# Optimization experiments

Measured on AMD Instinct MI355X. Metric: run time of the kernel, lower is better.

## Reference

```python
import jax, jax.numpy as jnp
import numpy as np

TOKENS, HIDDEN = 2048, 1024
N_EXPERTS, INTER, TOPK = 8, 2816, 2
RENORMALIZE = True


def setup_inputs() -> dict:
    key = jax.random.key(0)
    k1, k2, k3, k4 = jax.random.split(key, 4)
    x = jax.random.normal(k1, (TOKENS, HIDDEN), dtype=jnp.float32)
    gating_output = jax.random.normal(k2, (TOKENS, N_EXPERTS), dtype=jnp.float32)
    # stacked gate_proj+up_proj per expert: [E, 2*I, H]
    w1 = jax.random.normal(k3, (N_EXPERTS, 2 * INTER, HIDDEN), dtype=jnp.float32) * 0.02
    # down_proj per expert: [E, H, I]
    w2 = jax.random.normal(k4, (N_EXPERTS, HIDDEN, INTER), dtype=jnp.float32) * 0.02
    return {"x": x, "gating_output": gating_output, "w1": w1, "w2": w2}


def _moe(x, gating_output, w1, w2):
    # fused_topk: softmax over router logits, then top-k, then renormalize
    probs = jax.nn.softmax(gating_output, axis=-1)              # [T, E]
    topk_w, topk_ids = jax.lax.top_k(probs, TOPK)                # [T, K]
    if RENORMALIZE:
        topk_w = topk_w / jnp.sum(topk_w, axis=-1, keepdims=True)
    # fused_experts: gate/up proj -> SiLU(gate)*up -> down proj, per expert
    h = jnp.einsum('th,eih->tei', x, w1)                         # [T, E, 2I]
    gate, up = h[..., :INTER], h[..., INTER:]
    act = jax.nn.silu(gate) * up                                 # [T, E, I]
    out_e = jnp.einsum('tei,ehi->teh', act, w2)                  # [T, E, H]
    # combine: gather selected experts and weight them
    sel = jnp.take_along_axis(out_e, topk_ids[:, :, None], axis=1)  # [T, K, H]
    return jnp.sum(sel * topk_w[:, :, None].astype(sel.dtype), axis=1)  # [T, H]


def reference(x, gating_output, w1, w2):
    return _moe(x, gating_output, w1, w2)
```

## Files before the change

### kernel.cpp

```cpp
#include <hip/hip_runtime.h>
#include <hip/hip_bf16.h>

#define TOKENS 2048
#define HIDDEN 1024
#define NEXP   8
#define INTER  2816
#define N1     5632
#define ROWCAP 5120
#define MT     40
#define NT1    44
#define NT2    8
#define SPLITK 2

typedef __attribute__((ext_vector_type(8))) short short8;
typedef __attribute__((ext_vector_type(4))) float f32x4;

typedef unsigned int __attribute__((address_space(1))) as1_uint;
typedef unsigned int __attribute__((address_space(3))) as3_uint;

__device__ __forceinline__ void gload16(const void* g, void* l) {
  __builtin_amdgcn_global_load_lds((const as1_uint*)g, (as3_uint*)l, 16, 0, 0);
}

__device__ __forceinline__ unsigned short f2bf(float f) {
  unsigned u = __float_as_uint(f);
  u += 0x7fff + ((u >> 16) & 1);
  return (unsigned short)(u >> 16);
}
__device__ __forceinline__ float bf2f(unsigned short h) {
  return __uint_as_float(((unsigned)h) << 16);
}
__device__ __forceinline__ unsigned short bfs(float x) {
  __hip_bfloat16 h = __float2bfloat16(x);
  return *reinterpret_cast<unsigned short*>(&h);
}
__device__ __forceinline__ short8 pack8(f32x4 lo, f32x4 hi) {
  short8 o;
  o[0] = (short)bfs(lo[0]); o[1] = (short)bfs(lo[1]); o[2] = (short)bfs(lo[2]); o[3] = (short)bfs(lo[3]);
  o[4] = (short)bfs(hi[0]); o[5] = (short)bfs(hi[1]); o[6] = (short)bfs(hi[2]); o[7] = (short)bfs(hi[3]);
  return o;
}

__global__ void k_routing(const float* __restrict__ gate, int* __restrict__ ctrl,
                          int* __restrict__ tkid, float* __restrict__ tkw) {
  int t = blockIdx.x * blockDim.x + threadIdx.x;
  if (t >= TOKENS) return;
  float l[8];
#pragma unroll
  for (int i = 0; i < 8; i++) l[i] = gate[t * 8 + i];
  int i0 = 0; float m0 = l[0];
#pragma unroll
  for (int i = 1; i < 8; i++) if (l[i] > m0) { m0 = l[i]; i0 = i; }
  int i1 = -1; float m1 = -3.4e38f;
#pragma unroll
  for (int i = 0; i < 8; i++) if (i != i0 && l[i] > m1) { m1 = l[i]; i1 = i; }
  float e  = __expf(m1 - m0);
  float w0 = 1.f / (1.f + e);
  float w1 = e / (1.f + e);
  tkid[2 * t] = i0; tkid[2 * t + 1] = i1;
  tkw[2 * t] = w0;  tkw[2 * t + 1] = w1;
  atomicAdd(&ctrl[i0], 1);
  atomicAdd(&ctrl[i1], 1);
}

__global__ void k_base(int* ctrl) {
  if (threadIdx.x == 0) {
    int a = 0;
    for (int e = 0; e < 8; e++) { ctrl[16 + e] = a; a += ((ctrl[e] + 127) >> 7) << 7; }
  }
}

__global__ void k_fill(int* __restrict__ ctrl, const int* __restrict__ tkid,
                       int* __restrict__ rtok, int* __restrict__ trow) {
  int t = blockIdx.x * blockDim.x + threadIdx.x;
  if (t >= TOKENS) return;
#pragma unroll
  for (int k = 0; k < 2; k++) {
    int e = tkid[2 * t + k];
    int pos = atomicAdd(&ctrl[8 + e], 1);
    int row = ctrl[16 + e] + pos;
    rtok[row] = t;
    trow[2 * t + k] = row;
  }
}

__global__ void k_gather(const float* __restrict__ x, const int* __restrict__ ctrl,
                         const int* __restrict__ rtok, unsigned short* __restrict__ Abf) {
  int row = blockIdx.x;
  int e = -1, local = 0;
  for (int i = 0; i < 8; i++) {
    int b = ctrl[16 + i], p = ((ctrl[i] + 127) >> 7) << 7;
    if (row >= b && row < b + p) { e = i; local = row - b; break; }
  }
  if (e < 0) return;
  int tid = threadIdx.x;
  unsigned short* dst = Abf + (size_t)row * HIDDEN;
  if (local < ctrl[e]) {
    int t = rtok[row];
    float4 v = ((const float4*)(x + (size_t)t * HIDDEN))[tid];
    ushort4 o; o.x = f2bf(v.x); o.y = f2bf(v.y); o.z = f2bf(v.z); o.w = f2bf(v.w);
    ((ushort4*)dst)[tid] = o;
  } else {
    ushort4 z; z.x = 0; z.y = 0; z.z = 0; z.w = 0;
    ((ushort4*)dst)[tid] = z;
  }
}

__device__ __forceinline__ int tile_lookup(const int* ctrl, int mt, int* ml) {
  int a0 = 0;
  for (int i = 0; i < 8; i++) {
    int pt = (ctrl[i] + 127) >> 7;
    if (mt < a0 + pt) { *ml = mt - a0; return i; }
    a0 += pt;
  }
  return -1;
}

__global__ __launch_bounds__(256, 3) void k_gemm1(const float* __restrict__ w1,
    const unsigned short* __restrict__ Abf, unsigned short* __restrict__ act,
    const int* __restrict__ ctrl) {
  union __align__(16) LdsU {
    struct { unsigned char A[16384]; unsigned char Bf[32768]; } st;
    unsigned short hb[128 * 132];
  };
  __shared__ LdsU lds;
  int bid = blockIdx.x;
  int wg = (bid & 7) * (NT1 * MT / 8) + (bid >> 3);
  int nt = wg / MT, mt = wg % MT;
  int ml; int e = tile_lookup(ctrl, mt, &ml);
  if (e < 0) return;
  int tid = threadIdx.x, lane = tid & 63, wid = tid >> 6, wr = wid >> 1, wc = wid & 1;
  int rbase = ctrl[16 + e] + ml * 128;
  const unsigned char* Ab = (const unsigned char*)(Abf + (size_t)rbase * HIDDEN);
  const unsigned char* Bw = (const unsigned char*)(w1 + (size_t)e * N1 * HIDDEN);
  int l3 = lane >> 3, l4 = lane >> 4, l15 = lane & 15;
  int swzA = ((lane & 7) ^ l3) << 4;

  unsigned aoff[4], boff[8];
#pragma unroll
  for (int i = 0; i < 4; i++) {
    int g = wid * 4 + i;
    aoff[i] = (unsigned)(g * 8 + l3) * (HIDDEN * 2) + swzA;
  }
#pragma unroll
  for (int i = 0; i < 8; i++) {
    int r = (wid * 8 + i) * 4 + l4;
    int grow = (r < 64) ? nt * 64 + r : INTER + nt * 64 + (r - 64);
    boff[i] = (unsigned)grow * (HIDDEN * 4) + ((l15 ^ (r & 15)) << 4);
  }

  f32x4 acc[4][4];
  f32x4 zero = {0.f, 0.f, 0.f, 0.f};
#pragma unroll
  for (int i = 0; i < 4; i++)
#pragma unroll
    for (int j = 0; j < 4; j++) acc[i][j] = zero;

  for (int kk = 0; kk < HIDDEN / 64; ++kk) {
#pragma unroll
    for (int i = 0; i < 4; i++)
      gload16(Ab + (size_t)aoff[i] + kk * 128, &lds.st.A[(wid * 4 + i) * 1024]);
#pragma unroll
    for (int i = 0; i < 8; i++)
      gload16(Bw + (size_t)boff[i] + kk * 256, &lds.st.Bf[(wid * 8 + i) * 1024]);
    __syncthreads();
#pragma unroll
    for (int ks = 0; ks < 2; ++ks) {
      short8 a[4], b[4];
#pragma unroll
      for (int mi = 0; mi < 4; mi++) {
        int row = wr * 64 + mi * 16 + l15;
        int koff = ks * 64 + (l4 << 4);
        a[mi] = *(const short8*)&lds.st.A[row * 128 + (koff ^ ((row & 7) << 4))];
      }
#pragma unroll
      for (int ni = 0; ni < 4; ni++) {
        int r = wc * 64 + ni * 16 + l15;
        int c = ks * 8 + l4 * 2;
        f32x4 lo = *(const f32x4*)&lds.st.Bf[r * 256 + ((c ^ (r & 15)) << 4)];
        f32x4 hi = *(const f32x4*)&lds.st.Bf[r * 256 + (((c + 1) ^ (r & 15)) << 4)];
        b[ni] = pack8(lo, hi);
      }
#pragma unroll
      for (int mi = 0; mi < 4; mi++)
#pragma unroll
        for (int ni = 0; ni < 4; ni++)
          acc[mi][ni] = __builtin_amdgcn_mfma_f32_16x16x32_bf16(a[mi], b[ni], acc[mi][ni], 0, 0, 0);
    }
    __syncthreads();
  }
#pragma unroll
  for (int mi = 0; mi < 4; mi++)
#pragma unroll
    for (int ni = 0; ni < 4; ni++)
#pragma unroll
      for (int r = 0; r < 4; r++) {
        int row = wr * 64 + mi * 16 + (l4 << 2) + r;
        int col = wc * 64 + ni * 16 + l15;
        lds.hb[row * 132 + col] = f2bf(acc[mi][ni][r]);
      }
  __syncthreads();
  {
    int r = tid >> 1, ch = (tid & 1) * 32;
    unsigned short* orow = act + (size_t)(rbase + r) * INTER + nt * 64 + ch;
    const unsigned short* hrow = &lds.hb[r * 132];
#pragma unroll
    for (int j = 0; j < 32; j += 4) {
      ushort4 o;
#pragma unroll
      for (int q = 0; q < 4; q++) {
        float g = bf2f(hrow[ch + j + q]);
        float u = bf2f(hrow[64 + ch + j + q]);
        float s = g / (1.f + __expf(-g));
        ((unsigned short*)&o)[q] = f2bf(s * u);
      }
      *(ushort4*)(orow + j) = o;
    }
  }
}

__global__ __launch_bounds__(256, 3) void k_gemm2(const float* __restrict__ w2,
    const unsigned short* __restrict__ act, float* __restrict__ Pb,
    const int* __restrict__ ctrl) {
  struct __align__(16) Lds2 { unsigned char A[16384]; unsigned char Bf[32768]; };
  __shared__ Lds2 lds;
  int bid = blockIdx.x;
  int wg = (bid & 7) * (NT2 * MT * SPLITK / 8) + (bid >> 3);
  int mt = wg % MT;
  int p = wg / MT;
  int z = p & 1, nt = p >> 1;
  int ml; int e = tile_lookup(ctrl, mt, &ml);
  if (e < 0) return;
  int tid = threadIdx.x, lane = tid & 63, wid = tid >> 6, wr = wid >> 1, wc = wid & 1;
  int rbase = ctrl[16 + e] + ml * 128;
  const int KST = (INTER / 64) / SPLITK;
  const unsigned char* Ab = (const unsigned char*)(act + (size_t)rbase * INTER) + (size_t)z * KST * 128;
  const unsigned char* Bw = (const unsigned char*)(w2 + (size_t)e * HIDDEN * INTER) + (size_t)z * KST * 256;
  int l3 = lane >> 3, l4 = lane >> 4, l15 = lane & 15;
  int swzA = ((lane & 7) ^ l3) << 4;

  unsigned aoff[4], boff[8];
#pragma unroll
  for (int i = 0; i < 4; i++) {
    int g = wid * 4 + i;
    aoff[i] = (unsigned)(g * 8 + l3) * (INTER * 2) + swzA;
  }
#pragma unroll
  for (int i = 0; i < 8; i++) {
    int r = (wid * 8 + i) * 4 + l4;
    boff[i] = (unsigned)(nt * 128 + r) * (INTER * 4) + ((l15 ^ (r & 15)) << 4);
  }

  f32x4 acc[4][4];
  f32x4 zero = {0.f, 0.f, 0.f, 0.f};
#pragma unroll
  for (int i = 0; i < 4; i++)
#pragma unroll
    for (int j = 0; j < 4; j++) acc[i][j] = zero;

  for (int s = 0; s < KST; ++s) {
#pragma unroll
    for (int i = 0; i < 4; i++)
      gload16(Ab + (size_t)aoff[i] + s * 128, &lds.A[(wid * 4 + i) * 1024]);
#pragma unroll
    for (int i = 0; i < 8; i++)
      gload16(Bw + (size_t)boff[i] + s * 256, &lds.Bf[(wid * 8 + i) * 1024]);
    __syncthreads();
#pragma unroll
    for (int ks = 0; ks < 2; ++ks) {
      short8 a[4], b[4];
#pragma unroll
      for (int mi = 0; mi < 4; mi++) {
        int row = wr * 64 + mi * 16 + l15;
        int koff = ks * 64 + (l4 << 4);
        a[mi] = *(const short8*)&lds.A[row * 128 + (koff ^ ((row & 7) << 4))];
      }
#pragma unroll
      for (int ni = 0; ni < 4; ni++) {
        int r = wc * 64 + ni * 16 + l15;
        int c = ks * 8 + l4 * 2;
        f32x4 lo = *(const f32x4*)&lds.Bf[r * 256 + ((c ^ (r & 15)) << 4)];
        f32x4 hi = *(const f32x4*)&lds.Bf[r * 256 + (((c + 1) ^ (r & 15)) << 4)];
        b[ni] = pack8(lo, hi);
      }
#pragma unroll
      for (int mi = 0; mi < 4; mi++)
#pragma unroll
        for (int ni = 0; ni < 4; ni++)
          acc[mi][ni] = __builtin_amdgcn_mfma_f32_16x16x32_bf16(a[mi], b[ni], acc[mi][ni], 0, 0, 0);
    }
    __syncthreads();
  }
  float* P = Pb + (size_t)z * ROWCAP * HIDDEN;
#pragma unroll
  for (int mi = 0; mi < 4; mi++)
#pragma unroll
    for (int ni = 0; ni < 4; ni++) {
      int col = nt * 128 + wc * 64 + ni * 16 + l15;
#pragma unroll
      for (int r = 0; r < 4; r++) {
        int row = rbase + wr * 64 + mi * 16 + (l4 << 2) + r;
        P[(size_t)row * HIDDEN + col] = acc[mi][ni][r];
      }
    }
}

__global__ void k_finish(const float* __restrict__ Pb,
                         const int* __restrict__ trow, const float* __restrict__ tkw,
                         float* __restrict__ out) {
  int t = blockIdx.x, c = threadIdx.x;
  const float* P0 = Pb;
  const float* P1 = Pb + (size_t)ROWCAP * HIDDEN;
  int r0 = trow[2 * t], r1 = trow[2 * t + 1];
  float w0 = tkw[2 * t], w1 = tkw[2 * t + 1];
  float4 a0 = ((const float4*)(P0 + (size_t)r0 * HIDDEN))[c];
  float4 b0 = ((const float4*)(P1 + (size_t)r0 * HIDDEN))[c];
  float4 a1 = ((const float4*)(P0 + (size_t)r1 * HIDDEN))[c];
  float4 b1 = ((const float4*)(P1 + (size_t)r1 * HIDDEN))[c];
  float4 o;
  o.x = w0 * (a0.x + b0.x) + w1 * (a1.x + b1.x);
  o.y = w0 * (a0.y + b0.y) + w1 * (a1.y + b1.y);
  o.z = w0 * (a0.z + b0.z) + w1 * (a1.z + b1.z);
  o.w = w0 * (a0.w + b0.w) + w1 * (a1.w + b1.w);
  ((float4*)(out + (size_t)t * HIDDEN))[c] = o;
}

extern "C" void kernel_launch(void* const* d_in, const int* in_sizes, int n_in,
                              void* d_out, int out_size, void* d_ws, size_t ws_size,
                              hipStream_t stream) {
  const float* x      = (const float*)d_in[0];
  const float* gating = (const float*)d_in[1];
  const float* w1     = (const float*)d_in[2];
  const float* w2     = (const float*)d_in[3];
  float* out = (float*)d_out;
  char* ws = (char*)d_ws;

  int*   ctrl = (int*)ws;
  int*   tkid = (int*)(ws + 4096);
  float* tkw  = (float*)(ws + 24576);
  int*   rtok = (int*)(ws + 45056);
  int*   trow = (int*)(ws + 73728);
  size_t off_Abf = 131072;
  size_t off_act = off_Abf + (size_t)ROWCAP * HIDDEN * 2;
  size_t off_P   = off_act + (size_t)ROWCAP * INTER * 2;
  unsigned short* Abf  = (unsigned short*)(ws + off_Abf);
  unsigned short* actb = (unsigned short*)(ws + off_act);
  float* Pb = (float*)(ws + off_P);

  hipMemsetAsync(ws, 0, 1024, stream);

  k_routing<<<TOKENS / 256, 256, 0, stream>>>(gating, ctrl, tkid, tkw);
  k_base<<<1, 64, 0, stream>>>(ctrl);
  k_fill<<<TOKENS / 256, 256, 0, stream>>>(ctrl, tkid, rtok, trow);
  k_gather<<<ROWCAP, 256, 0, stream>>>(x, ctrl, rtok, Abf);
  k_gemm1<<<NT1 * MT, 256, 0, stream>>>(w1, Abf, actb, ctrl);
  k_gemm2<<<NT2 * MT * SPLITK, 256, 0, stream>>>(w2, actb, Pb, ctrl);
  k_finish<<<TOKENS, 256, 0, stream>>>(Pb, trow, tkw, out);
}
```

Baseline: 239.2 us.

## Use 256-row M tiles with 512 threads and double-buffered LDS in expert GEMMs

Both expert GEMMs now use 256-row M tiles with 8 waves per block, and expert row padding is raised to 256 to match (ROWCAP 6144, MT 24). The K loop is restructured into a two-stage LDS ping-pong, so the next slab's global-to-LDS loads are issued while MFMAs run on the current one. This aims to hide load latency and to reuse each weight tile across twice as many rows. In exchange, the larger padding adds wasted rows of compute, and the 128KB LDS footprint limits each CU to one block, so occupancy drops.

```diff
diff --git a/kernel.cpp b/kernel.cpp
--- a/kernel.cpp
+++ b/kernel.cpp
@@ -6,8 +6,8 @@
 #define NEXP   8
 #define INTER  2816
 #define N1     5632
-#define ROWCAP 5120
-#define MT     40
+#define ROWCAP 6144
+#define MT     24
 #define NT1    44
 #define NT2    8
 #define SPLITK 2
@@ -66,7 +66,7 @@
 __global__ void k_base(int* ctrl) {
   if (threadIdx.x == 0) {
     int a = 0;
-    for (int e = 0; e < 8; e++) { ctrl[16 + e] = a; a += ((ctrl[e] + 127) >> 7) << 7; }
+    for (int e = 0; e < 8; e++) { ctrl[16 + e] = a; a += ((ctrl[e] + 255) >> 8) << 8; }
   }
 }
 
@@ -89,7 +89,7 @@
   int row = blockIdx.x;
   int e = -1, local = 0;
   for (int i = 0; i < 8; i++) {
-    int b = ctrl[16 + i], p = ((ctrl[i] + 127) >> 7) << 7;
+    int b = ctrl[16 + i], p = ((ctrl[i] + 255) >> 8) << 8;
     if (row >= b && row < b + p) { e = i; local = row - b; break; }
   }
   if (e < 0) return;
@@ -109,19 +109,20 @@
 __device__ __forceinline__ int tile_lookup(const int* ctrl, int mt, int* ml) {
   int a0 = 0;
   for (int i = 0; i < 8; i++) {
-    int pt = (ctrl[i] + 127) >> 7;
+    int pt = (ctrl[i] + 255) >> 8;
     if (mt < a0 + pt) { *ml = mt - a0; return i; }
     a0 += pt;
   }
   return -1;
 }
 
-__global__ __launch_bounds__(256, 3) void k_gemm1(const float* __restrict__ w1,
+__global__ __launch_bounds__(512, 2) void k_gemm1(const float* __restrict__ w1,
     const unsigned short* __restrict__ Abf, unsigned short* __restrict__ act,
     const int* __restrict__ ctrl) {
   union __align__(16) LdsU {
-    struct { unsigned char A[16384]; unsigned char Bf[32768]; } st;
-    unsigned short hb[128 * 132];
+    struct { unsigned char A0[32768]; unsigned char Bf0[32768];
+             unsigned char A1[32768]; unsigned char Bf1[32768]; } st;
+    unsigned short hb[256 * 132];
   };
   __shared__ LdsU lds;
   int bid = blockIdx.x;
@@ -130,21 +131,21 @@
   int ml; int e = tile_lookup(ctrl, mt, &ml);
   if (e < 0) return;
   int tid = threadIdx.x, lane = tid & 63, wid = tid >> 6, wr = wid >> 1, wc = wid & 1;
-  int rbase = ctrl[16 + e] + ml * 128;
+  int rbase = ctrl[16 + e] + ml * 256;
   const unsigned char* Ab = (const unsigned char*)(Abf + (size_t)rbase * HIDDEN);
   const unsigned char* Bw = (const unsigned char*)(w1 + (size_t)e * N1 * HIDDEN);
   int l3 = lane >> 3, l4 = lane >> 4, l15 = lane & 15;
   int swzA = ((lane & 7) ^ l3) << 4;
 
-  unsigned aoff[4], boff[8];
+  unsigned aoff[4], boff[4];
 #pragma unroll
   for (int i = 0; i < 4; i++) {
     int g = wid * 4 + i;
     aoff[i] = (unsigned)(g * 8 + l3) * (HIDDEN * 2) + swzA;
   }
 #pragma unroll
-  for (int i = 0; i < 8; i++) {
-    int r = (wid * 8 + i) * 4 + l4;
+  for (int i = 0; i < 4; i++) {
+    int r = (wid * 4 + i) * 4 + l4;
     int grow = (r < 64) ? nt * 64 + r : INTER + nt * 64 + (r - 64);
     boff[i] = (unsigned)grow * (HIDDEN * 4) + ((l15 ^ (r & 15)) << 4);
   }
@@ -156,39 +157,48 @@
 #pragma unroll
     for (int j = 0; j < 4; j++) acc[i][j] = zero;
 
-  for (int kk = 0; kk < HIDDEN / 64; ++kk) {
-#pragma unroll
-    for (int i = 0; i < 4; i++)
-      gload16(Ab + (size_t)aoff[i] + kk * 128, &lds.st.A[(wid * 4 + i) * 1024]);
-#pragma unroll
-    for (int i = 0; i < 8; i++)
-      gload16(Bw + (size_t)boff[i] + kk * 256, &lds.st.Bf[(wid * 8 + i) * 1024]);
+#define STG1(kk, Ad, Bd) do {                                                        \
+  _Pragma("unroll") for (int i = 0; i < 4; i++)                                      \
+    gload16(Ab + (size_t)aoff[i] + (kk) * 128, &(Ad)[(wid * 4 + i) * 1024]);         \
+  _Pragma("unroll") for (int i = 0; i < 4; i++)                                      \
+    gload16(Bw + (size_t)boff[i] + (kk) * 256, &(Bd)[(wid * 4 + i) * 1024]);         \
+} while (0)
+
+#define CMP1(Ad, Bd) do {                                                            \
+  _Pragma("unroll") for (int ks = 0; ks < 2; ++ks) {                                 \
+    short8 a[4], b[4];                                                               \
+    _Pragma("unroll") for (int mi = 0; mi < 4; mi++) {                               \
+      int row = wr * 64 + mi * 16 + l15;                                             \
+      int koff = ks * 64 + (l4 << 4);                                                \
+      a[mi] = *(const short8*)&(Ad)[row * 128 + (koff ^ ((row & 7) << 4))];          \
+    }                                                                                \
+    _Pragma("unroll") for (int ni = 0; ni < 4; ni++) {                               \
+      int r = wc * 64 + ni * 16 + l15;                                               \
+      int c = ks * 8 + l4 * 2;                                                       \
+      f32x4 lo = *(const f32x4*)&(Bd)[r * 256 + ((c ^ (r & 15)) << 4)];              \
+      f32x4 hi = *(const f32x4*)&(Bd)[r * 256 + (((c + 1) ^ (r & 15)) << 4)];        \
+      b[ni] = pack8(lo, hi);                                                         \
+    }                                                                                \
+    _Pragma("unroll") for (int mi = 0; mi < 4; mi++)                                 \
+      _Pragma("unroll") for (int ni = 0; ni < 4; ni++)                               \
+        acc[mi][ni] = __builtin_amdgcn_mfma_f32_16x16x32_bf16(a[mi], b[ni], acc[mi][ni], 0, 0, 0); \
+  }                                                                                  \
+} while (0)
+
+  const int NS = HIDDEN / 64;
+  STG1(0, lds.st.A0, lds.st.Bf0);
+  __syncthreads();
+  for (int s = 0; s < NS; s += 2) {
+    STG1(s + 1, lds.st.A1, lds.st.Bf1);
+    CMP1(lds.st.A0, lds.st.Bf0);
     __syncthreads();
-#pragma unroll
-    for (int ks = 0; ks < 2; ++ks) {
-      short8 a[4], b[4];
-#pragma unroll
-      for (int mi = 0; mi < 4; mi++) {
-        int row = wr * 64 + mi * 16 + l15;
-        int koff = ks * 64 + (l4 << 4);
-        a[mi] = *(const short8*)&lds.st.A[row * 128 + (koff ^ ((row & 7) << 4))];
-      }
-#pragma unroll
-      for (int ni = 0; ni < 4; ni++) {
-        int r = wc * 64 + ni * 16 + l15;
-        int c = ks * 8 + l4 * 2;
-        f32x4 lo = *(const f32x4*)&lds.st.Bf[r * 256 + ((c ^ (r & 15)) << 4)];
-        f32x4 hi = *(const f32x4*)&lds.st.Bf[r * 256 + (((c + 1) ^ (r & 15)) << 4)];
-        b[ni] = pack8(lo, hi);
-      }
-#pragma unroll
-      for (int mi = 0; mi < 4; mi++)
-#pragma unroll
-        for (int ni = 0; ni < 4; ni++)
-          acc[mi][ni] = __builtin_amdgcn_mfma_f32_16x16x32_bf16(a[mi], b[ni], acc[mi][ni], 0, 0, 0);
-    }
+    if (s + 2 < NS) STG1(s + 2, lds.st.A0, lds.st.Bf0);
+    CMP1(lds.st.A1, lds.st.Bf1);
     __syncthreads();
   }
+#undef STG1
+#undef CMP1
+
 #pragma unroll
   for (int mi = 0; mi < 4; mi++)
 #pragma unroll
@@ -219,10 +229,11 @@
   }
 }
 
-__global__ __launch_bounds__(256, 3) void k_gemm2(const float* __restrict__ w2,
+__global__ __launch_bounds__(512, 2) void k_gemm2(const float* __restrict__ w2,
     const unsigned short* __restrict__ act, float* __restrict__ Pb,
     const int* __restrict__ ctrl) {
-  struct __align__(16) Lds2 { unsigned char A[16384]; unsigned char Bf[32768]; };
+  struct __align__(16) Lds2 { unsigned char A0[32768]; unsigned char Bf0[32768];
+                              unsigned char A1[32768]; unsigned char Bf1[32768]; };
   __shared__ Lds2 lds;
   int bid = blockIdx.x;
   int wg = (bid & 7) * (NT2 * MT * SPLITK / 8) + (bid >> 3);
@@ -232,22 +243,22 @@
   int ml; int e = tile_lookup(ctrl, mt, &ml);
   if (e < 0) return;
   int tid = threadIdx.x, lane = tid & 63, wid = tid >> 6, wr = wid >> 1, wc = wid & 1;
-  int rbase = ctrl[16 + e] + ml * 128;
+  int rbase = ctrl[16 + e] + ml * 256;
   const int KST = (INTER / 64) / SPLITK;
   const unsigned char* Ab = (const unsigned char*)(act + (size_t)rbase * INTER) + (size_t)z * KST * 128;
   const unsigned char* Bw = (const unsigned char*)(w2 + (size_t)e * HIDDEN * INTER) + (size_t)z * KST * 256;
   int l3 = lane >> 3, l4 = lane >> 4, l15 = lane & 15;
   int swzA = ((lane & 7) ^ l3) << 4;
 
-  unsigned aoff[4], boff[8];
+  unsigned aoff[4], boff[4];
 #pragma unroll
   for (int i = 0; i < 4; i++) {
     int g = wid * 4 + i;
     aoff[i] = (unsigned)(g * 8 + l3) * (INTER * 2) + swzA;
   }
 #pragma unroll
-  for (int i = 0; i < 8; i++) {
-    int r = (wid * 8 + i) * 4 + l4;
+  for (int i = 0; i < 4; i++) {
+    int r = (wid * 4 + i) * 4 + l4;
     boff[i] = (unsigned)(nt * 128 + r) * (INTER * 4) + ((l15 ^ (r & 15)) << 4);
   }
 
@@ -258,39 +269,47 @@
 #pragma unroll
     for (int j = 0; j < 4; j++) acc[i][j] = zero;
 
-  for (int s = 0; s < KST; ++s) {
-#pragma unroll
-    for (int i = 0; i < 4; i++)
-      gload16(Ab + (size_t)aoff[i] + s * 128, &lds.A[(wid * 4 + i) * 1024]);
-#pragma unroll
-    for (int i = 0; i < 8; i++)
-      gload16(Bw + (size_t)boff[i] + s * 256, &lds.Bf[(wid * 8 + i) * 1024]);
+#define STG2(kk, Ad, Bd) do {                                                        \
+  _Pragma("unroll") for (int i = 0; i < 4; i++)                                      \
+    gload16(Ab + (size_t)aoff[i] + (kk) * 128, &(Ad)[(wid * 4 + i) * 1024]);         \
+  _Pragma("unroll") for (int i = 0; i < 4; i++)                                      \
+    gload16(Bw + (size_t)boff[i] + (kk) * 256, &(Bd)[(wid * 4 + i) * 1024]);         \
+} while (0)
+
+#define CMP2(Ad, Bd) do {                                                            \
+  _Pragma("unroll") for (int ks = 0; ks < 2; ++ks) {                                 \
+    short8 a[4], b[4];                                                               \
+    _Pragma("unroll") for (int mi = 0; mi < 4; mi++) {                               \
+      int row = wr * 64 + mi * 16 + l15;                                             \
+      int koff = ks * 64 + (l4 << 4);                                                \
+      a[mi] = *(const short8*)&(Ad)[row * 128 + (koff ^ ((row & 7) << 4))];          \
+    }                                                                                \
+    _Pragma("unroll") for (int ni = 0; ni < 4; ni++) {                               \
+      int r = wc * 64 + ni * 16 + l15;                                               \
+      int c = ks * 8 + l4 * 2;                                                       \
+      f32x4 lo = *(const f32x4*)&(Bd)[r * 256 + ((c ^ (r & 15)) << 4)];              \
+      f32x4 hi = *(const f32x4*)&(Bd)[r * 256 + (((c + 1) ^ (r & 15)) << 4)];        \
+      b[ni] = pack8(lo, hi);                                                         \
+    }                                                                                \
+    _Pragma("unroll") for (int mi = 0; mi < 4; mi++)                                 \
+      _Pragma("unroll") for (int ni = 0; ni < 4; ni++)                               \
+        acc[mi][ni] = __builtin_amdgcn_mfma_f32_16x16x32_bf16(a[mi], b[ni], acc[mi][ni], 0, 0, 0); \
+  }                                                                                  \
+} while (0)
+
+  STG2(0, lds.A0, lds.Bf0);
+  __syncthreads();
+  for (int s = 0; s < KST; s += 2) {
+    STG2(s + 1, lds.A1, lds.Bf1);
+    CMP2(lds.A0, lds.Bf0);
     __syncthreads();
-#pragma unroll
-    for (int ks = 0; ks < 2; ++ks) {
-      short8 a[4], b[4];
-#pragma unroll
-      for (int mi = 0; mi < 4; mi++) {
-        int row = wr * 64 + mi * 16 + l15;
-        int koff = ks * 64 + (l4 << 4);
-        a[mi] = *(const short8*)&lds.A[row * 128 + (koff ^ ((row & 7) << 4))];
-      }
-#pragma unroll
-      for (int ni = 0; ni < 4; ni++) {
-        int r = wc * 64 + ni * 16 + l15;
-        int c = ks * 8 + l4 * 2;
-        f32x4 lo = *(const f32x4*)&lds.Bf[r * 256 + ((c ^ (r & 15)) << 4)];
-        f32x4 hi = *(const f32x4*)&lds.Bf[r * 256 + (((c + 1) ^ (r & 15)) << 4)];
-        b[ni] = pack8(lo, hi);
-      }
-#pragma unroll
-      for (int mi = 0; mi < 4; mi++)
-#pragma unroll
-        for (int ni = 0; ni < 4; ni++)
-          acc[mi][ni] = __builtin_amdgcn_mfma_f32_16x16x32_bf16(a[mi], b[ni], acc[mi][ni], 0, 0, 0);
-    }
+    if (s + 2 < KST) STG2(s + 2, lds.A0, lds.Bf0);
+    CMP2(lds.A1, lds.Bf1);
     __syncthreads();
   }
+#undef STG2
+#undef CMP2
+
   float* P = Pb + (size_t)z * ROWCAP * HIDDEN;
 #pragma unroll
   for (int mi = 0; mi < 4; mi++)
@@ -353,7 +372,7 @@
   k_base<<<1, 64, 0, stream>>>(ctrl);
   k_fill<<<TOKENS / 256, 256, 0, stream>>>(ctrl, tkid, rtok, trow);
   k_gather<<<ROWCAP, 256, 0, stream>>>(x, ctrl, rtok, Abf);
-  k_gemm1<<<NT1 * MT, 256, 0, stream>>>(w1, Abf, actb, ctrl);
-  k_gemm2<<<NT2 * MT * SPLITK, 256, 0, stream>>>(w2, actb, Pb, ctrl);
+  k_gemm1<<<NT1 * MT, 512, 0, stream>>>(w1, Abf, actb, ctrl);
+  k_gemm2<<<NT2 * MT * SPLITK, 512, 0, stream>>>(w2, actb, Pb, ctrl);
   k_finish<<<TOKENS, 256, 0, stream>>>(Pb, trow, tkw, out);
 }
```

After: 277.4 us. 16.0% more time.

## Pre-convert expert weights to bf16 before the expert GEMMs

Applied to the files above, without the earlier changes.

Adds a grid-stride conversion kernel that turns w1 and w2 from fp32 to bf16 in workspace on every call. Both GEMMs then load bf16 B tiles directly with the same swizzled layout as A, so the per-MFMA fp32-to-bf16 packing disappears. B tiles shrink to half the LDS, which allows launch bounds of 4 blocks per CU. The cost is an extra full pass over all weights each call: a fp32 read plus a bf16 write. The split-K partial buffer is aliased onto the w1 bf16 region, which gemm1 has already finished reading by the time gemm2 writes there.

```diff
diff --git a/kernel.cpp b/kernel.cpp
--- a/kernel.cpp
+++ b/kernel.cpp
@@ -30,15 +30,18 @@
 __device__ __forceinline__ float bf2f(unsigned short h) {
   return __uint_as_float(((unsigned)h) << 16);
 }
-__device__ __forceinline__ unsigned short bfs(float x) {
-  __hip_bfloat16 h = __float2bfloat16(x);
-  return *reinterpret_cast<unsigned short*>(&h);
-}
-__device__ __forceinline__ short8 pack8(f32x4 lo, f32x4 hi) {
-  short8 o;
-  o[0] = (short)bfs(lo[0]); o[1] = (short)bfs(lo[1]); o[2] = (short)bfs(lo[2]); o[3] = (short)bfs(lo[3]);
-  o[4] = (short)bfs(hi[0]); o[5] = (short)bfs(hi[1]); o[6] = (short)bfs(hi[2]); o[7] = (short)bfs(hi[3]);
-  return o;
+
+__global__ void k_conv(const float* __restrict__ src, unsigned short* __restrict__ dst, int n8) {
+  int i = blockIdx.x * blockDim.x + threadIdx.x;
+  int stride = gridDim.x * blockDim.x;
+  for (; i < n8; i += stride) {
+    float4 a = ((const float4*)src)[2 * i];
+    float4 b = ((const float4*)src)[2 * i + 1];
+    union { ushort us[8]; uint4 v; } o;
+    o.us[0] = f2bf(a.x); o.us[1] = f2bf(a.y); o.us[2] = f2bf(a.z); o.us[3] = f2bf(a.w);
+    o.us[4] = f2bf(b.x); o.us[5] = f2bf(b.y); o.us[6] = f2bf(b.z); o.us[7] = f2bf(b.w);
+    ((uint4*)dst)[i] = o.v;
+  }
 }
 
 __global__ void k_routing(const float* __restrict__ gate, int* __restrict__ ctrl,
@@ -116,11 +119,11 @@
   return -1;
 }
 
-__global__ __launch_bounds__(256, 3) void k_gemm1(const float* __restrict__ w1,
+__global__ __launch_bounds__(256, 4) void k_gemm1b(const unsigned short* __restrict__ w1b,
     const unsigned short* __restrict__ Abf, unsigned short* __restrict__ act,
     const int* __restrict__ ctrl) {
   union __align__(16) LdsU {
-    struct { unsigned char A[16384]; unsigned char Bf[32768]; } st;
+    struct { unsigned char A[16384]; unsigned char B[16384]; } st;
     unsigned short hb[128 * 132];
   };
   __shared__ LdsU lds;
@@ -132,21 +135,18 @@
   int tid = threadIdx.x, lane = tid & 63, wid = tid >> 6, wr = wid >> 1, wc = wid & 1;
   int rbase = ctrl[16 + e] + ml * 128;
   const unsigned char* Ab = (const unsigned char*)(Abf + (size_t)rbase * HIDDEN);
-  const unsigned char* Bw = (const unsigned char*)(w1 + (size_t)e * N1 * HIDDEN);
+  const unsigned char* Bb = (const unsigned char*)(w1b + (size_t)e * N1 * HIDDEN);
   int l3 = lane >> 3, l4 = lane >> 4, l15 = lane & 15;
-  int swzA = ((lane & 7) ^ l3) << 4;
-
-  unsigned aoff[4], boff[8];
+  int swz = ((lane & 7) ^ l3) << 4;
+
+  unsigned aoff[4], boff[4];
 #pragma unroll
   for (int i = 0; i < 4; i++) {
     int g = wid * 4 + i;
-    aoff[i] = (unsigned)(g * 8 + l3) * (HIDDEN * 2) + swzA;
-  }
-#pragma unroll
-  for (int i = 0; i < 8; i++) {
-    int r = (wid * 8 + i) * 4 + l4;
-    int grow = (r < 64) ? nt * 64 + r : INTER + nt * 64 + (r - 64);
-    boff[i] = (unsigned)grow * (HIDDEN * 4) + ((l15 ^ (r & 15)) << 4);
+    aoff[i] = (unsigned)(g * 8 + l3) * (HIDDEN * 2) + swz;
+    int r0 = g * 8;
+    int grow = (r0 < 64) ? (nt * 64 + r0 + l3) : (INTER + nt * 64 + r0 - 64 + l3);
+    boff[i] = (unsigned)grow * (HIDDEN * 2) + swz;
   }
 
   f32x4 acc[4][4];
@@ -161,8 +161,8 @@
     for (int i = 0; i < 4; i++)
       gload16(Ab + (size_t)aoff[i] + kk * 128, &lds.st.A[(wid * 4 + i) * 1024]);
 #pragma unroll
-    for (int i = 0; i < 8; i++)
-      gload16(Bw + (size_t)boff[i] + kk * 256, &lds.st.Bf[(wid * 8 + i) * 1024]);
+    for (int i = 0; i < 4; i++)
+      gload16(Bb + (size_t)boff[i] + kk * 128, &lds.st.B[(wid * 4 + i) * 1024]);
     __syncthreads();
 #pragma unroll
     for (int ks = 0; ks < 2; ++ks) {
@@ -175,11 +175,9 @@
       }
 #pragma unroll
       for (int ni = 0; ni < 4; ni++) {
-        int r = wc * 64 + ni * 16 + l15;
-        int c = ks * 8 + l4 * 2;
-        f32x4 lo = *(const f32x4*)&lds.st.Bf[r * 256 + ((c ^ (r & 15)) << 4)];
-        f32x4 hi = *(const f32x4*)&lds.st.Bf[r * 256 + (((c + 1) ^ (r & 15)) << 4)];
-        b[ni] = pack8(lo, hi);
+        int row = wc * 64 + ni * 16 + l15;
+        int koff = ks * 64 + (l4 << 4);
+        b[ni] = *(const short8*)&lds.st.B[row * 128 + (koff ^ ((row & 7) << 4))];
       }
 #pragma unroll
       for (int mi = 0; mi < 4; mi++)
@@ -219,10 +217,10 @@
   }
 }
 
-__global__ __launch_bounds__(256, 3) void k_gemm2(const float* __restrict__ w2,
+__global__ __launch_bounds__(256, 4) void k_gemm2b(const unsigned short* __restrict__ w2b,
     const unsigned short* __restrict__ act, float* __restrict__ Pb,
     const int* __restrict__ ctrl) {
-  struct __align__(16) Lds2 { unsigned char A[16384]; unsigned char Bf[32768]; };
+  struct __align__(16) Lds2 { unsigned char A[16384]; unsigned char B[16384]; };
   __shared__ Lds2 lds;
   int bid = blockIdx.x;
   int wg = (bid & 7) * (NT2 * MT * SPLITK / 8) + (bid >> 3);
@@ -235,20 +233,16 @@
   int rbase = ctrl[16 + e] + ml * 128;
   const int KST = (INTER / 64) / SPLITK;
   const unsigned char* Ab = (const unsigned char*)(act + (size_t)rbase * INTER) + (size_t)z * KST * 128;
-  const unsigned char* Bw = (const unsigned char*)(w2 + (size_t)e * HIDDEN * INTER) + (size_t)z * KST * 256;
+  const unsigned char* Bb = (const unsigned char*)(w2b + (size_t)e * HIDDEN * INTER) + (size_t)z * KST * 128;
   int l3 = lane >> 3, l4 = lane >> 4, l15 = lane & 15;
-  int swzA = ((lane & 7) ^ l3) << 4;
-
-  unsigned aoff[4], boff[8];
+  int swz = ((lane & 7) ^ l3) << 4;
+
+  unsigned aoff[4], boff[4];
 #pragma unroll
   for (int i = 0; i < 4; i++) {
     int g = wid * 4 + i;
-    aoff[i] = (unsigned)(g * 8 + l3) * (INTER * 2) + swzA;
-  }
-#pragma unroll
-  for (int i = 0; i < 8; i++) {
-    int r = (wid * 8 + i) * 4 + l4;
-    boff[i] = (unsigned)(nt * 128 + r) * (INTER * 4) + ((l15 ^ (r & 15)) << 4);
+    aoff[i] = (unsigned)(g * 8 + l3) * (INTER * 2) + swz;
+    boff[i] = (unsigned)(nt * 128 + g * 8 + l3) * (INTER * 2) + swz;
   }
 
   f32x4 acc[4][4];
@@ -258,13 +252,13 @@
 #pragma unroll
     for (int j = 0; j < 4; j++) acc[i][j] = zero;
 
-  for (int s = 0; s < KST; ++s) {
+  for (int kk = 0; kk < KST; ++kk) {
 #pragma unroll
     for (int i = 0; i < 4; i++)
-      gload16(Ab + (size_t)aoff[i] + s * 128, &lds.A[(wid * 4 + i) * 1024]);
-#pragma unroll
-    for (int i = 0; i < 8; i++)
-      gload16(Bw + (size_t)boff[i] + s * 256, &lds.Bf[(wid * 8 + i) * 1024]);
+      gload16(Ab + (size_t)aoff[i] + kk * 128, &lds.A[(wid * 4 + i) * 1024]);
+#pragma unroll
+    for (int i = 0; i < 4; i++)
+      gload16(Bb + (size_t)boff[i] + kk * 128, &lds.B[(wid * 4 + i) * 1024]);
     __syncthreads();
 #pragma unroll
     for (int ks = 0; ks < 2; ++ks) {
@@ -277,11 +271,9 @@
       }
 #pragma unroll
       for (int ni = 0; ni < 4; ni++) {
-        int r = wc * 64 + ni * 16 + l15;
-        int c = ks * 8 + l4 * 2;
-        f32x4 lo = *(const f32x4*)&lds.Bf[r * 256 + ((c ^ (r & 15)) << 4)];
-        f32x4 hi = *(const f32x4*)&lds.Bf[r * 256 + (((c + 1) ^ (r & 15)) << 4)];
-        b[ni] = pack8(lo, hi);
+        int row = wc * 64 + ni * 16 + l15;
+        int koff = ks * 64 + (l4 << 4);
+        b[ni] = *(const short8*)&lds.B[row * 128 + (koff ^ ((row & 7) << 4))];
       }
 #pragma unroll
       for (int mi = 0; mi < 4; mi++)
@@ -342,18 +334,23 @@
   int*   trow = (int*)(ws + 73728);
   size_t off_Abf = 131072;
   size_t off_act = off_Abf + (size_t)ROWCAP * HIDDEN * 2;
-  size_t off_P   = off_act + (size_t)ROWCAP * INTER * 2;
+  size_t off_w2b = off_act + (size_t)ROWCAP * INTER * 2;
+  size_t off_w1b = off_w2b + (size_t)NEXP * HIDDEN * INTER * 2;
   unsigned short* Abf  = (unsigned short*)(ws + off_Abf);
   unsigned short* actb = (unsigned short*)(ws + off_act);
-  float* Pb = (float*)(ws + off_P);
+  unsigned short* w2b  = (unsigned short*)(ws + off_w2b);
+  unsigned short* w1b  = (unsigned short*)(ws + off_w1b);
+  float* Pb = (float*)(ws + off_w1b);
 
   hipMemsetAsync(ws, 0, 1024, stream);
 
+  k_conv<<<2048, 256, 0, stream>>>(w1, w1b, NEXP * N1 * HIDDEN / 8);
+  k_conv<<<2048, 256, 0, stream>>>(w2, w2b, NEXP * HIDDEN * INTER / 8);
   k_routing<<<TOKENS / 256, 256, 0, stream>>>(gating, ctrl, tkid, tkw);
   k_base<<<1, 64, 0, stream>>>(ctrl);
   k_fill<<<TOKENS / 256, 256, 0, stream>>>(ctrl, tkid, rtok, trow);
   k_gather<<<ROWCAP, 256, 0, stream>>>(x, ctrl, rtok, Abf);
-  k_gemm1<<<NT1 * MT, 256, 0, stream>>>(w1, Abf, actb, ctrl);
-  k_gemm2<<<NT2 * MT * SPLITK, 256, 0, stream>>>(w2, actb, Pb, ctrl);
+  k_gemm1b<<<NT1 * MT, 256, 0, stream>>>(w1b, Abf, actb, ctrl);
+  k_gemm2b<<<NT2 * MT * SPLITK, 256, 0, stream>>>(w2b, actb, Pb, ctrl);
   k_finish<<<TOKENS, 256, 0, stream>>>(Pb, trow, tkw, out);
 }
```

New measurement: 259.3 us. +8.4%, slower.

## Pre-convert w2 to bf16 in the gather kernel and use bf16 B tiles in gemm2

Applied to the files above, without the earlier changes.

The gather kernel gains extra blocks that convert the whole fp32 down-projection weight tensor to bf16 in a workspace buffer. The second GEMM then loads bf16 B tiles with the same swizzled layout as the A operand, so each MMA input is loaded directly instead of packing two fp32 vectors. This halves the B-operand LDS footprint, which allows raising the launch-bounds occupancy to 4. The cost is a full pass that reads all fp32 w2 and writes a bf16 copy on every call, plus extra workspace memory.

```diff
diff --git a/kernel.cpp b/kernel.cpp
--- a/kernel.cpp
+++ b/kernel.cpp
@@ -11,6 +11,7 @@
 #define NT1    44
 #define NT2    8
 #define SPLITK 2
+#define CONVB  2048
 
 typedef __attribute__((ext_vector_type(8))) short short8;
 typedef __attribute__((ext_vector_type(4))) float f32x4;
@@ -84,25 +85,41 @@
   }
 }
 
-__global__ void k_gather(const float* __restrict__ x, const int* __restrict__ ctrl,
-                         const int* __restrict__ rtok, unsigned short* __restrict__ Abf) {
-  int row = blockIdx.x;
-  int e = -1, local = 0;
-  for (int i = 0; i < 8; i++) {
-    int b = ctrl[16 + i], p = ((ctrl[i] + 127) >> 7) << 7;
-    if (row >= b && row < b + p) { e = i; local = row - b; break; }
-  }
-  if (e < 0) return;
-  int tid = threadIdx.x;
-  unsigned short* dst = Abf + (size_t)row * HIDDEN;
-  if (local < ctrl[e]) {
-    int t = rtok[row];
-    float4 v = ((const float4*)(x + (size_t)t * HIDDEN))[tid];
-    ushort4 o; o.x = f2bf(v.x); o.y = f2bf(v.y); o.z = f2bf(v.z); o.w = f2bf(v.w);
-    ((ushort4*)dst)[tid] = o;
+__global__ void k_prep(const float* __restrict__ x, const int* __restrict__ ctrl,
+                       const int* __restrict__ rtok, unsigned short* __restrict__ Abf,
+                       const float* __restrict__ w2, unsigned short* __restrict__ w2b) {
+  int b = blockIdx.x;
+  if (b < ROWCAP) {
+    int row = b;
+    int e = -1, local = 0;
+    for (int i = 0; i < 8; i++) {
+      int bb = ctrl[16 + i], p = ((ctrl[i] + 127) >> 7) << 7;
+      if (row >= bb && row < bb + p) { e = i; local = row - bb; break; }
+    }
+    if (e < 0) return;
+    int tid = threadIdx.x;
+    unsigned short* dst = Abf + (size_t)row * HIDDEN;
+    if (local < ctrl[e]) {
+      int t = rtok[row];
+      float4 v = ((const float4*)(x + (size_t)t * HIDDEN))[tid];
+      ushort4 o; o.x = f2bf(v.x); o.y = f2bf(v.y); o.z = f2bf(v.z); o.w = f2bf(v.w);
+      ((ushort4*)dst)[tid] = o;
+    } else {
+      ushort4 z; z.x = 0; z.y = 0; z.z = 0; z.w = 0;
+      ((ushort4*)dst)[tid] = z;
+    }
   } else {
-    ushort4 z; z.x = 0; z.y = 0; z.z = 0; z.w = 0;
-    ((ushort4*)dst)[tid] = z;
+    const int n8 = NEXP * HIDDEN * INTER / 8;
+    int i = (b - ROWCAP) * blockDim.x + threadIdx.x;
+    int stride = CONVB * blockDim.x;
+    for (; i < n8; i += stride) {
+      float4 a = ((const float4*)w2)[2 * i];
+      float4 c = ((const float4*)w2)[2 * i + 1];
+      union { ushort us[8]; uint4 v; } o;
+      o.us[0] = f2bf(a.x); o.us[1] = f2bf(a.y); o.us[2] = f2bf(a.z); o.us[3] = f2bf(a.w);
+      o.us[4] = f2bf(c.x); o.us[5] = f2bf(c.y); o.us[6] = f2bf(c.z); o.us[7] = f2bf(c.w);
+      ((uint4*)w2b)[i] = o.v;
+    }
   }
 }
 
@@ -219,10 +236,10 @@
   }
 }
 
-__global__ __launch_bounds__(256, 3) void k_gemm2(const float* __restrict__ w2,
+__global__ __launch_bounds__(256, 4) void k_gemm2b(const unsigned short* __restrict__ w2b,
     const unsigned short* __restrict__ act, float* __restrict__ Pb,
     const int* __restrict__ ctrl) {
-  struct __align__(16) Lds2 { unsigned char A[16384]; unsigned char Bf[32768]; };
+  struct __align__(16) Lds2 { unsigned char A[16384]; unsigned char B[16384]; };
   __shared__ Lds2 lds;
   int bid = blockIdx.x;
   int wg = (bid & 7) * (NT2 * MT * SPLITK / 8) + (bid >> 3);
@@ -235,20 +252,16 @@
   int rbase = ctrl[16 + e] + ml * 128;
   const int KST = (INTER / 64) / SPLITK;
   const unsigned char* Ab = (const unsigned char*)(act + (size_t)rbase * INTER) + (size_t)z * KST * 128;
-  const unsigned char* Bw = (const unsigned char*)(w2 + (size_t)e * HIDDEN * INTER) + (size_t)z * KST * 256;
+  const unsigned char* Bb = (const unsigned char*)(w2b + (size_t)e * HIDDEN * INTER) + (size_t)z * KST * 128;
   int l3 = lane >> 3, l4 = lane >> 4, l15 = lane & 15;
-  int swzA = ((lane & 7) ^ l3) << 4;
-
-  unsigned aoff[4], boff[8];
+  int swz = ((lane & 7) ^ l3) << 4;
+
+  unsigned aoff[4], boff[4];
 #pragma unroll
   for (int i = 0; i < 4; i++) {
     int g = wid * 4 + i;
-    aoff[i] = (unsigned)(g * 8 + l3) * (INTER * 2) + swzA;
-  }
-#pragma unroll
-  for (int i = 0; i < 8; i++) {
-    int r = (wid * 8 + i) * 4 + l4;
-    boff[i] = (unsigned)(nt * 128 + r) * (INTER * 4) + ((l15 ^ (r & 15)) << 4);
+    aoff[i] = (unsigned)(g * 8 + l3) * (INTER * 2) + swz;
+    boff[i] = (unsigned)(nt * 128 + g * 8 + l3) * (INTER * 2) + swz;
   }
 
   f32x4 acc[4][4];
@@ -258,13 +271,13 @@
 #pragma unroll
     for (int j = 0; j < 4; j++) acc[i][j] = zero;
 
-  for (int s = 0; s < KST; ++s) {
+  for (int kk = 0; kk < KST; ++kk) {
 #pragma unroll
     for (int i = 0; i < 4; i++)
-      gload16(Ab + (size_t)aoff[i] + s * 128, &lds.A[(wid * 4 + i) * 1024]);
-#pragma unroll
-    for (int i = 0; i < 8; i++)
-      gload16(Bw + (size_t)boff[i] + s * 256, &lds.Bf[(wid * 8 + i) * 1024]);
+      gload16(Ab + (size_t)aoff[i] + kk * 128, &lds.A[(wid * 4 + i) * 1024]);
+#pragma unroll
+    for (int i = 0; i < 4; i++)
+      gload16(Bb + (size_t)boff[i] + kk * 128, &lds.B[(wid * 4 + i) * 1024]);
     __syncthreads();
 #pragma unroll
     for (int ks = 0; ks < 2; ++ks) {
@@ -277,11 +290,9 @@
       }
 #pragma unroll
       for (int ni = 0; ni < 4; ni++) {
-        int r = wc * 64 + ni * 16 + l15;
-        int c = ks * 8 + l4 * 2;
-        f32x4 lo = *(const f32x4*)&lds.Bf[r * 256 + ((c ^ (r & 15)) << 4)];
-        f32x4 hi = *(const f32x4*)&lds.Bf[r * 256 + (((c + 1) ^ (r & 15)) << 4)];
-        b[ni] = pack8(lo, hi);
+        int row = wc * 64 + ni * 16 + l15;
+        int koff = ks * 64 + (l4 << 4);
+        b[ni] = *(const short8*)&lds.B[row * 128 + (koff ^ ((row & 7) << 4))];
       }
 #pragma unroll
       for (int mi = 0; mi < 4; mi++)
@@ -342,9 +353,11 @@
   int*   trow = (int*)(ws + 73728);
   size_t off_Abf = 131072;
   size_t off_act = off_Abf + (size_t)ROWCAP * HIDDEN * 2;
-  size_t off_P   = off_act + (size_t)ROWCAP * INTER * 2;
+  size_t off_w2b = off_act + (size_t)ROWCAP * INTER * 2;
+  size_t off_P   = off_w2b + (size_t)NEXP * HIDDEN * INTER * 2;
   unsigned short* Abf  = (unsigned short*)(ws + off_Abf);
   unsigned short* actb = (unsigned short*)(ws + off_act);
+  unsigned short* w2b  = (unsigned short*)(ws + off_w2b);
   float* Pb = (float*)(ws + off_P);
 
   hipMemsetAsync(ws, 0, 1024, stream);
@@ -352,8 +365,8 @@
   k_routing<<<TOKENS / 256, 256, 0, stream>>>(gating, ctrl, tkid, tkw);
   k_base<<<1, 64, 0, stream>>>(ctrl);
   k_fill<<<TOKENS / 256, 256, 0, stream>>>(ctrl, tkid, rtok, trow);
-  k_gather<<<ROWCAP, 256, 0, stream>>>(x, ctrl, rtok, Abf);
+  k_prep<<<ROWCAP + CONVB, 256, 0, stream>>>(x, ctrl, rtok, Abf, w2, w2b);
   k_gemm1<<<NT1 * MT, 256, 0, stream>>>(w1, Abf, actb, ctrl);
-  k_gemm2<<<NT2 * MT * SPLITK, 256, 0, stream>>>(w2, actb, Pb, ctrl);
+  k_gemm2b<<<NT2 * MT * SPLITK, 256, 0, stream>>>(w2b, actb, Pb, ctrl);
   k_finish<<<TOKENS, 256, 0, stream>>>(Pb, trow, tkw, out);
 }
```

Result: slower. 246.4 us (+3.0%).
